# Kernel tuning notes

Hardware: AMD Instinct MI355X
Metric: run time of the kernel (lower is better)

Reference implementation:

```python
import jax, jax.numpy as jnp
import numpy as np
import math

NUM_GRIDS = 128
INPUT_DIM = 128
OUTPUT_DIM = 128
BATCH = 8192
INIT_SCALE = 0.1


def _borders_cdf_grid(n_chunks):
    # inverse Laplace CDF grid borders, exactly as in the torch module
    def inv(u):
        return np.log(2.0 * u) if u <= 0.5 else -np.log(2.0 * (1.0 - u))
    cs = 1.0 / n_chunks
    b = [inv(i * cs) for i in range(1, n_chunks)]
    left = b[0] - (b[1] - b[0])
    right = b[-1] + (b[-1] - b[-2])
    return np.array([left] + b + [right], dtype=np.float32)  # [n_chunks+1]


def setup_inputs() -> dict:
    key = jax.random.key(0)
    kx, kp = jax.random.split(key)
    x = jax.random.normal(kx, (INPUT_DIM, BATCH), dtype=jnp.float32)
    s = INIT_SCALE / math.sqrt(INPUT_DIM)
    func_parameter = jax.random.uniform(
        kp, (NUM_GRIDS + 1, OUTPUT_DIM, INPUT_DIM), dtype=jnp.float32,
        minval=-s, maxval=s)
    borders = jnp.asarray(_borders_cdf_grid(NUM_GRIDS))
    inverse_chunk_lengths = 1.0 / (borders[1:] - borders[:-1])  # [NUM_GRIDS]
    return {"x": x, "func_parameter": func_parameter,
            "borders": borders, "inverse_chunk_lengths": inverse_chunk_lengths}


def reference(x, func_parameter, borders, inverse_chunk_lengths):
    # x: [I, B]; func_parameter: [G+1, O, I]
    G = borders.shape[0] - 1
    I = x.shape[0]
    # Laplace CDF: R -> [0, 1]
    exp_na = jnp.exp(-jnp.abs(x))
    cdf = jnp.where(x > 0, 1.0 - 0.5 * exp_na, 0.5 * exp_na)
    # bucketize on uniform CDF grid (truncation == floor since cdf*G >= 0)
    idx = jnp.clip((cdf * G).astype(jnp.int32), 0, G - 1)        # [I, B]
    idx_next = jnp.clip(idx + 1, 0, G)                           # [I, B]
    left = borders[idx]                                          # [I, B]
    inv_len = inverse_chunk_lengths[idx]                         # [I, B]
    d = (x - left) * inv_len                                     # [I, B]
    # gather per-input-dim parameter rows: val[i, b, o] = P[idx[i,b], o, i]
    Pt = jnp.transpose(func_parameter, (2, 0, 1))                # [I, G+1, O]
    rows = jnp.arange(I)[:, None]                                # [I, 1]
    val_l = Pt[rows, idx]                                        # [I, B, O]
    val_r = Pt[rows, idx_next]                                   # [I, B, O]
    out = ((1.0 - d)[..., None] * val_l + d[..., None] * val_r).sum(axis=0)  # [B, O]
    return out.T                                                 # [O, B]
```

## Files before the change

### kernel.cpp

```cpp
#include <hip/hip_runtime.h>
#include <cstdint>


#define NG 128
#define NI 128
#define NO 128
#define NB 8192

using half2v  = __attribute__((ext_vector_type(2))) _Float16;
using float4v = __attribute__((ext_vector_type(4))) float;

__device__ inline uint32_t pack_f16x2(float lo, float hi) {
    _Float16 hl = (_Float16)lo, hh = (_Float16)hi;
    return (uint32_t)__builtin_bit_cast(unsigned short, hl) |
           ((uint32_t)__builtin_bit_cast(unsigned short, hh) << 16);
}

__device__ inline void load_lds16(const uint32_t* g, uint32_t* l) {
    __builtin_amdgcn_global_load_lds(
        (const __attribute__((address_space(1))) uint32_t*)g,
        (__attribute__((address_space(3))) uint32_t*)l, 16, 0, 0);
}

__global__ __launch_bounds__(256) void build_q(const float* __restrict__ P,
                                               uint32_t* __restrict__ Q2) {
    __shared__ float L[5][16][128];
    const int gb = blockIdx.x >> 3;
    const int ob = blockIdx.x & 7;
    const int g0 = gb * 4;
    const int o0 = ob * 16;
    const int s0 = ob * 4;
    const int t  = threadIdx.x;
    #pragma unroll
    for (int pass = 0; pass < 40; ++pass) {
        int row = pass * 2 + (t >> 7);
        int i   = t & 127;
        int gg  = row >> 4, ol = row & 15;
        L[gg][ol][i] = P[(size_t)(g0 + gg) * (NO * NI) + (o0 + ol) * NI + i];
    }
    __syncthreads();
    #pragma unroll
    for (int pp = 0; pp < 2; ++pp) {
        int item = pp * 256 + t;
        int i  = item & 127;
        int sl = item >> 7;
        uint32_t* dst = Q2 + ((size_t)((s0 + sl) * NI + i) * NG + g0) * 4;
        #pragma unroll
        for (int gg = 0; gg < 4; ++gg) {
            uint32_t r[4];
            #pragma unroll
            for (int ow = 0; ow < 4; ++ow) {
                float pl = L[gg][sl * 4 + ow][i];
                float dd = L[gg + 1][sl * 4 + ow][i] - pl;
                r[ow] = pack_f16x2(pl, dd);
            }
            *(uint4*)(dst + gg * 4) = make_uint4(r[0], r[1], r[2], r[3]);
        }
    }
}

__global__ __launch_bounds__(256) void build_t(const float* __restrict__ x,
                                               const float* __restrict__ borders,
                                               const float* __restrict__ icl,
                                               uint32_t* __restrict__ T) {
    const int e0 = (blockIdx.x * 256 + threadIdx.x) * 4;
    const float4 xv = *(const float4*)(x + e0);
    uint32_t r[4];
    const float xs[4] = {xv.x, xv.y, xv.z, xv.w};
    #pragma unroll
    for (int k = 0; k < 4; ++k) {
        float v = xs[k];
        float ea = __expf(-fabsf(v));
        float cdf = v > 0.f ? 1.f - 0.5f * ea : 0.5f * ea;
        int idx = (int)(cdf * 128.f);
        idx = idx > 127 ? 127 : idx;
        float d = (v - borders[idx]) * icl[idx];
        _Float16 hd = (_Float16)d;
        r[k] = ((uint32_t)idx << 4) |
               ((uint32_t)__builtin_bit_cast(unsigned short, hd) << 16);
    }
    *(uint4*)(T + e0) = make_uint4(r[0], r[1], r[2], r[3]);
}

__global__ __launch_bounds__(1024, 8) void main_k(const uint32_t* __restrict__ Q2,
                                                  const uint32_t* __restrict__ T,
                                                  float* __restrict__ part) {
    __shared__ __align__(16) uint32_t slab[32 * NG * 4];
    const int t    = threadIdx.x;
    const int bx   = blockIdx.x;
    const int xcd  = bx & 7;
    const int s    = (bx >> 3) & 31;
    const int widx = bx >> 8;
    const int iq   = ((widx << 3) | xcd) >> 3;
    const int bt   = xcd;
    const int bme  = (bt << 10) | t;
    const uint32_t* Qs = Q2 + ((size_t)s * NI + iq * 32) * (NG * 4);
    const uint32_t* Tb = T + (size_t)(iq * 32) * NB + bme;

    #pragma unroll
    for (int k = 0; k < 4; ++k)
        load_lds16(Qs + (size_t)(t + k * 1024) * 4, &slab[(t + k * 1024) * 4]);
    uint32_t tt[16];
    #pragma unroll
    for (int il = 0; il < 16; ++il)
        tt[il] = Tb[(size_t)il * NB];
    __syncthreads();

    float a0 = 0.f, a1 = 0.f, a2 = 0.f, a3 = 0.f;
    #pragma unroll
    for (int ic = 0; ic < 2; ++ic) {
        uint32_t tn[16];
        if (ic == 0) {
            #pragma unroll
            for (int il = 0; il < 16; ++il)
                tn[il] = Tb[(size_t)(16 + il) * NB];
        }
        const char* sp = (const char*)slab + ic * 32768;
        #pragma unroll
        for (int il = 0; il < 16; ++il) {
            uint32_t tw  = tt[il];
            uint32_t off = tw & 0xFFFFu;
            uint32_t w2b = (tw & 0xFFFF0000u) | 0x3C00u;
            uint4 q = *(const uint4*)(sp + il * 2048 + off);
            half2v w2 = __builtin_bit_cast(half2v, w2b);
            a0 = __builtin_amdgcn_fdot2(__builtin_bit_cast(half2v, q.x), w2, a0, false);
            a1 = __builtin_amdgcn_fdot2(__builtin_bit_cast(half2v, q.y), w2, a1, false);
            a2 = __builtin_amdgcn_fdot2(__builtin_bit_cast(half2v, q.z), w2, a2, false);
            a3 = __builtin_amdgcn_fdot2(__builtin_bit_cast(half2v, q.w), w2, a3, false);
        }
        if (ic == 0) {
            #pragma unroll
            for (int il = 0; il < 16; ++il)
                tt[il] = tn[il];
        }
    }

    float* po = part + (size_t)iq * (NO * NB) + (size_t)(s * 4) * NB + bme;
    po[0]              = a0;
    po[NB]             = a1;
    po[2 * (size_t)NB] = a2;
    po[3 * (size_t)NB] = a3;
}

__global__ __launch_bounds__(256) void reduce_k(const float* __restrict__ part,
                                                float* __restrict__ out) {
    const int e0 = (blockIdx.x * 256 + threadIdx.x) * 4;
    const size_t st = (size_t)NO * NB;
    const float4v v0 = *(const float4v*)(part + e0);
    const float4v v1 = *(const float4v*)(part + st + e0);
    const float4v v2 = *(const float4v*)(part + 2 * st + e0);
    const float4v v3 = *(const float4v*)(part + 3 * st + e0);
    const float4v r  = (v0 + v1) + (v2 + v3);
    __builtin_nontemporal_store(r, (float4v*)(out + e0));
}

extern "C" void kernel_launch(void* const* d_in, const int* in_sizes, int n_in,
                              void* d_out, int out_size, void* d_ws, size_t ws_size,
                              hipStream_t stream) {
    const float* x       = (const float*)d_in[0];
    const float* P       = (const float*)d_in[1];
    const float* borders = (const float*)d_in[2];
    const float* icl     = (const float*)d_in[3];
    float* out = (float*)d_out;

    uint32_t* Q2  = (uint32_t*)d_ws;
    uint32_t* T   = Q2 + (size_t)NO * NI * NG;
    float*    prt = (float*)(T + (size_t)NI * NB);

    hipLaunchKernelGGL(build_q, dim3(256), dim3(256), 0, stream, P, Q2);
    hipLaunchKernelGGL(build_t, dim3(NI * NB / 1024), dim3(256), 0, stream,
                       x, borders, icl, T);
    hipLaunchKernelGGL(main_k, dim3(1024), dim3(1024), 0, stream, Q2, T, prt);
    hipLaunchKernelGGL(reduce_k, dim3(NO * NB / 1024), dim3(256), 0, stream,
                       prt, out);
}
```

Before: 105.0 us.

## Process four batch columns per thread to amortize LDS slab loads

Main kernel now uses 512 blocks of 512 threads, with each thread handling four batch columns instead of one. This halves the number of blocks that each load the same 64KB parameter slab into LDS, so slab traffic is spread over more work. It also replaces the two-phase T prefetch with a per-input-dim software pipeline. Each thread keeps 16 accumulators, which raises register pressure and cuts the number of resident threads.

```diff
diff --git a/kernel.cpp b/kernel.cpp
--- a/kernel.cpp
+++ b/kernel.cpp
@@ -82,64 +82,63 @@
     *(uint4*)(T + e0) = make_uint4(r[0], r[1], r[2], r[3]);
 }
 
-__global__ __launch_bounds__(1024, 8) void main_k(const uint32_t* __restrict__ Q2,
-                                                  const uint32_t* __restrict__ T,
-                                                  float* __restrict__ part) {
+__global__ __launch_bounds__(512, 4) void main_k(const uint32_t* __restrict__ Q2,
+                                                 const uint32_t* __restrict__ T,
+                                                 float* __restrict__ part) {
     __shared__ __align__(16) uint32_t slab[32 * NG * 4];
     const int t    = threadIdx.x;
     const int bx   = blockIdx.x;
-    const int xcd  = bx & 7;
-    const int s    = (bx >> 3) & 31;
-    const int widx = bx >> 8;
-    const int iq   = ((widx << 3) | xcd) >> 3;
-    const int bt   = xcd;
-    const int bme  = (bt << 10) | t;
+    const int pair = bx & 15;
+    const int s    = bx >> 4;
+    const int iq   = pair >> 2;
+    const int bq   = pair & 3;
+    const int b0   = (bq << 11) | t;
     const uint32_t* Qs = Q2 + ((size_t)s * NI + iq * 32) * (NG * 4);
-    const uint32_t* Tb = T + (size_t)(iq * 32) * NB + bme;
+    const uint32_t* Tb = T + (size_t)(iq * 32) * NB + b0;
 
     #pragma unroll
-    for (int k = 0; k < 4; ++k)
-        load_lds16(Qs + (size_t)(t + k * 1024) * 4, &slab[(t + k * 1024) * 4]);
-    uint32_t tt[16];
-    #pragma unroll
-    for (int il = 0; il < 16; ++il)
-        tt[il] = Tb[(size_t)il * NB];
+    for (int k = 0; k < 8; ++k)
+        load_lds16(Qs + (size_t)(t + k * 512) * 4, &slab[(t + k * 512) * 4]);
+    uint32_t tw0 = Tb[0], tw1 = Tb[512], tw2 = Tb[1024], tw3 = Tb[1536];
     __syncthreads();
 
-    float a0 = 0.f, a1 = 0.f, a2 = 0.f, a3 = 0.f;
+    float acc[16];
     #pragma unroll
-    for (int ic = 0; ic < 2; ++ic) {
-        uint32_t tn[16];
-        if (ic == 0) {
-            #pragma unroll
-            for (int il = 0; il < 16; ++il)
-                tn[il] = Tb[(size_t)(16 + il) * NB];
+    for (int k = 0; k < 16; ++k) acc[k] = 0.f;
+
+    #pragma unroll
+    for (int i = 0; i < 32; ++i) {
+        uint32_t nw0, nw1, nw2, nw3;
+        if (i < 31) {
+            const uint32_t* tn = Tb + (size_t)(i + 1) * NB;
+            nw0 = tn[0]; nw1 = tn[512]; nw2 = tn[1024]; nw3 = tn[1536];
         }
-        const char* sp = (const char*)slab + ic * 32768;
+        const char* sp = (const char*)slab + i * 2048;
+        const uint32_t tws[4] = {tw0, tw1, tw2, tw3};
         #pragma unroll
-        for (int il = 0; il < 16; ++il) {
-            uint32_t tw  = tt[il];
-            uint32_t off = tw & 0xFFFFu;
+        for (int j = 0; j < 4; ++j) {
+            uint32_t tw  = tws[j];
+            uint4 q = *(const uint4*)(sp + (tw & 0xFFFFu));
             uint32_t w2b = (tw & 0xFFFF0000u) | 0x3C00u;
-            uint4 q = *(const uint4*)(sp + il * 2048 + off);
             half2v w2 = __builtin_bit_cast(half2v, w2b);
-            a0 = __builtin_amdgcn_fdot2(__builtin_bit_cast(half2v, q.x), w2, a0, false);
-            a1 = __builtin_amdgcn_fdot2(__builtin_bit_cast(half2v, q.y), w2, a1, false);
-            a2 = __builtin_amdgcn_fdot2(__builtin_bit_cast(half2v, q.z), w2, a2, false);
-            a3 = __builtin_amdgcn_fdot2(__builtin_bit_cast(half2v, q.w), w2, a3, false);
+            acc[j * 4 + 0] = __builtin_amdgcn_fdot2(
+                __builtin_bit_cast(half2v, q.x), w2, acc[j * 4 + 0], false);
+            acc[j * 4 + 1] = __builtin_amdgcn_fdot2(
+                __builtin_bit_cast(half2v, q.y), w2, acc[j * 4 + 1], false);
+            acc[j * 4 + 2] = __builtin_amdgcn_fdot2(
+                __builtin_bit_cast(half2v, q.z), w2, acc[j * 4 + 2], false);
+            acc[j * 4 + 3] = __builtin_amdgcn_fdot2(
+                __builtin_bit_cast(half2v, q.w), w2, acc[j * 4 + 3], false);
         }
-        if (ic == 0) {
-            #pragma unroll
-            for (int il = 0; il < 16; ++il)
-                tt[il] = tn[il];
-        }
+        if (i < 31) { tw0 = nw0; tw1 = nw1; tw2 = nw2; tw3 = nw3; }
     }
 
-    float* po = part + (size_t)iq * (NO * NB) + (size_t)(s * 4) * NB + bme;
-    po[0]              = a0;
-    po[NB]             = a1;
-    po[2 * (size_t)NB] = a2;
-    po[3 * (size_t)NB] = a3;
+    float* po = part + (size_t)iq * (NO * NB) + (size_t)(s * 4) * NB;
+    #pragma unroll
+    for (int j = 0; j < 4; ++j)
+        #pragma unroll
+        for (int ow = 0; ow < 4; ++ow)
+            po[(size_t)ow * NB + b0 + j * 512] = acc[j * 4 + ow];
 }
 
 __global__ __launch_bounds__(256) void reduce_k(const float* __restrict__ part,
@@ -170,7 +169,7 @@
     hipLaunchKernelGGL(build_q, dim3(256), dim3(256), 0, stream, P, Q2);
     hipLaunchKernelGGL(build_t, dim3(NI * NB / 1024), dim3(256), 0, stream,
                        x, borders, icl, T);
-    hipLaunchKernelGGL(main_k, dim3(1024), dim3(1024), 0, stream, Q2, T, prt);
+    hipLaunchKernelGGL(main_k, dim3(512), dim3(512), 0, stream, Q2, T, prt);
     hipLaunchKernelGGL(reduce_k, dim3(NO * NB / 1024), dim3(256), 0, stream,
                        prt, out);
 }
```

After: 108.1 us. 1.03x slower.
